# Kernel tuning notes

Hardware: AMD Instinct MI355X
Metric: run time of the kernel (lower is better)

The kernel has to match this reference:

```python
import jax, jax.numpy as jnp
import numpy as np

D_MODEL = 1024
D_STATE = 16
D_CONV = 4
EXPAND = 2
D_INNER = EXPAND * D_MODEL  # 2048
DT_MIN, DT_MAX = 0.001, 0.1
BATCH, SEQ = 4, 2048


def _silu(v):
    return v * jax.nn.sigmoid(v)


def setup_inputs() -> dict:
    key = jax.random.key(0)
    ks = jax.random.split(key, 5)
    x = jax.random.normal(ks[0], (BATCH, SEQ, D_MODEL), jnp.float32)
    W_in = jax.random.normal(ks[1], (2 * D_INNER, D_MODEL), jnp.float32) / np.sqrt(D_MODEL)
    conv_w = jax.random.normal(ks[2], (D_INNER, D_CONV), jnp.float32) / np.sqrt(D_CONV)
    conv_b = jnp.zeros((D_INNER,), jnp.float32)
    W_xproj = jax.random.normal(ks[3], (2 * D_STATE + 1, D_INNER), jnp.float32) / np.sqrt(D_INNER)
    A_log = jnp.log(jnp.arange(1, D_STATE + 1, dtype=jnp.float32))
    D_param = jnp.ones((D_INNER,), jnp.float32)
    W_out = jax.random.normal(ks[4], (D_MODEL, D_INNER), jnp.float32) / np.sqrt(D_INNER)
    return dict(x=x, W_in=W_in, conv_w=conv_w, conv_b=conv_b,
                W_xproj=W_xproj, A_log=A_log, D_param=D_param, W_out=W_out)


def reference(x, W_in, conv_w, conv_b, W_xproj, A_log, D_param, W_out):
    b, l, d = x.shape
    xz = x @ W_in.T                                   # (B, L, 2*d_inner)
    x_proj, z = jnp.split(xz, 2, axis=-1)             # each (B, L, d_inner)

    # Depthwise causal conv1d (kernel D_CONV, left-pad D_CONV-1, truncate to L)
    xp = jnp.pad(x_proj, ((0, 0), (D_CONV - 1, 0), (0, 0)))
    x_conv = conv_b + sum(xp[:, k:k + l, :] * conv_w[:, k] for k in range(D_CONV))
    x_conv = _silu(x_conv)                            # (B, L, d_inner)

    x_dbl = x_conv @ W_xproj.T                        # (B, L, 2*d_state+1)
    Bmat = x_dbl[..., :D_STATE]                       # (B, L, d_state)
    Cmat = x_dbl[..., D_STATE:2 * D_STATE]            # (B, L, d_state)
    dt = jnp.clip(jax.nn.softplus(x_dbl[..., -1]), DT_MIN, DT_MAX)  # (B, L)

    A = -jnp.exp(A_log)                               # (d_state,)

    def step(h, inp):
        x_t, dt_t, B_t, C_t = inp                     # (b,di), (b,), (b,ds), (b,ds)
        dt_A = jnp.clip(dt_t[:, None] * A, -20.0, 0.0)          # (b, ds)
        A_bar = jnp.exp(dt_A)[:, None, :]                        # (b, 1, ds)
        B_bar = jnp.clip(dt_t[:, None] * B_t, -10.0, 10.0)[:, None, :]
        h = jnp.clip(A_bar * h + B_bar * x_t[:, :, None], -100.0, 100.0)
        y_t = jnp.einsum('bds,bs->bd', h, C_t)
        return h, y_t

    h0 = jnp.zeros((b, D_INNER, D_STATE), x.dtype)
    xs = (jnp.swapaxes(x_conv, 0, 1), jnp.swapaxes(dt, 0, 1),
          jnp.swapaxes(Bmat, 0, 1), jnp.swapaxes(Cmat, 0, 1))
    _, ys = jax.lax.scan(step, h0, xs)                # ys: (L, B, d_inner)
    y = jnp.swapaxes(ys, 0, 1)                        # (B, L, d_inner)

    y = y * _silu(z) + x_conv * D_param
    return y @ W_out.T                                # (B, L, d_model)
```

## Files before the change

kernel.cpp:

```cpp
#include <hip/hip_runtime.h>
#include <cmath>

#define D_MODEL 1024
#define D_STATE 16
#define D_INNER 2048
#define NB 4
#define SEQL 2048
#define ROWS (NB*SEQL)
#define XZ_LD (2*D_INNER)

typedef __attribute__((ext_vector_type(8))) short short8;
typedef __attribute__((ext_vector_type(4))) float f32x4;

__device__ __forceinline__ float sigmoidf_(float v) { return 1.0f / (1.0f + __expf(-v)); }

__device__ __forceinline__ unsigned short bf16rne(float f) {
    unsigned u = __float_as_uint(f);
    unsigned r = (u + 0x7FFFu + ((u >> 16) & 1u)) >> 16;
    return (unsigned short)r;
}

__global__ __launch_bounds__(256) void pack1_k(const float4* __restrict__ in,
    ushort4* __restrict__ out, int n4)
{
    int i = blockIdx.x * 256 + threadIdx.x;
    if (i >= n4) return;
    float4 v = in[i];
    ushort4 h;
    h.x = bf16rne(v.x); h.y = bf16rne(v.y); h.z = bf16rne(v.z); h.w = bf16rne(v.w);
    out[i] = h;
}

#define GLDS(gp, lp) __builtin_amdgcn_global_load_lds( \
    (const __attribute__((address_space(1))) void*)(gp), \
    (__attribute__((address_space(3))) void*)(lp), 16, 0, 0)

extern __shared__ __align__(16) unsigned short smem8[];

template<int BM>
__global__ __launch_bounds__(512, 2) void gemm8p(
    const unsigned short* __restrict__ A2, int lda,
    const unsigned short* __restrict__ B2, int ldb,
    float* __restrict__ C, int ldc, int K)
{
    constexpr int APAN = BM * 32;
    constexpr int BPAN = 256 * 32;
    constexpr int LA   = BM / 128;
    constexpr int MH   = BM / 128;
    constexpr int WROW = (BM == 256) ? 128 : 64;
    unsigned short* sA = smem8;
    unsigned short* sB = smem8 + 3 * APAN;

    const int tid = threadIdx.x;
    const int bm = blockIdx.y * BM, bn = blockIdx.x * 256;
    const int wave = tid >> 6, lane = tid & 63;
    const int wm = wave >> 2, wn = wave & 3;
    const int fr = lane & 15, kq = lane >> 4;
    const int NT = K >> 5;

    size_t offA[LA], offB[2];
#pragma unroll
    for (int i = 0; i < LA; ++i) {
        int c = i * 512 + tid;
        int row = c & (BM - 1), slot = (BM == 256) ? (c >> 8) : (c >> 7);
        offA[i] = (size_t)(bm + row) * lda + slot * 8;
    }
#pragma unroll
    for (int i = 0; i < 2; ++i) {
        int c = i * 512 + tid;
        int row = c & 255, slot = c >> 8;
        offB[i] = (size_t)(bn + row) * ldb + slot * 8;
    }

    auto stageA = [&](int s) {
        int ka = s * 32;
        unsigned short* d = sA + (s % 3) * APAN;
#pragma unroll
        for (int i = 0; i < LA; ++i)
            GLDS(A2 + offA[i] + ka, d + (i * 512 + tid) * 8);
    };
    auto stageB = [&](int s) {
        int kb = s * 32;
        unsigned short* d = sB + (s % 3) * BPAN;
#pragma unroll
        for (int i = 0; i < 2; ++i)
            GLDS(B2 + offB[i] + kb, d + (i * 512 + tid) * 8);
    };

    f32x4 acc[4 * MH][4];
#pragma unroll
    for (int m = 0; m < 4 * MH; ++m)
#pragma unroll
        for (int n = 0; n < 4; ++n) acc[m][n] = (f32x4){0.f, 0.f, 0.f, 0.f};

    stageA(0); stageB(0); stageA(1); stageB(1);
    if constexpr (BM == 256) asm volatile("s_waitcnt vmcnt(4)" ::: "memory");
    else                     asm volatile("s_waitcnt vmcnt(3)" ::: "memory");
    __builtin_amdgcn_s_barrier();
    asm volatile("" ::: "memory");

    for (int t = 0; t < NT; ++t) {
        const unsigned short* pA = sA + (t % 3) * APAN;
        const unsigned short* pB = sB + (t % 3) * BPAN;
        short8 b0[4], a0[4];
#pragma unroll
        for (int n = 0; n < 4; ++n)
            b0[n] = *(const short8*)&pB[(kq * 256 + wn * 64 + n * 16 + fr) * 8];
#pragma unroll
        for (int m = 0; m < 4; ++m)
            a0[m] = *(const short8*)&pA[(kq * BM + wm * WROW + m * 16 + fr) * 8];
        if (t + 2 < NT) stageA(t + 2);
        if constexpr (MH == 1) { if (t + 2 < NT) stageB(t + 2); }
        __builtin_amdgcn_s_barrier();
        asm volatile("" ::: "memory");
        __builtin_amdgcn_s_setprio(1);
#pragma unroll
        for (int m = 0; m < 4; ++m)
#pragma unroll
            for (int n = 0; n < 4; ++n)
                acc[m][n] = __builtin_amdgcn_mfma_f32_16x16x32_bf16(a0[m], b0[n], acc[m][n], 0, 0, 0);
        __builtin_amdgcn_s_setprio(0);
        if constexpr (MH == 2) {
            __builtin_amdgcn_s_barrier();
            asm volatile("" ::: "memory");
            short8 a1[4];
#pragma unroll
            for (int m = 0; m < 4; ++m)
                a1[m] = *(const short8*)&pA[(kq * 256 + wm * 128 + 64 + m * 16 + fr) * 8];
            if (t + 2 < NT) stageB(t + 2);
            __builtin_amdgcn_s_barrier();
            asm volatile("" ::: "memory");
            __builtin_amdgcn_s_setprio(1);
#pragma unroll
            for (int m = 0; m < 4; ++m)
#pragma unroll
                for (int n = 0; n < 4; ++n)
                    acc[4 + m][n] = __builtin_amdgcn_mfma_f32_16x16x32_bf16(a1[m], b0[n], acc[4 + m][n], 0, 0, 0);
            __builtin_amdgcn_s_setprio(0);
        }
        if (t + 2 < NT) {
            if constexpr (BM == 256) asm volatile("s_waitcnt vmcnt(4)" ::: "memory");
            else                     asm volatile("s_waitcnt vmcnt(3)" ::: "memory");
        } else if (t + 1 < NT) {
            asm volatile("s_waitcnt vmcnt(0)" ::: "memory");
        }
        __builtin_amdgcn_s_barrier();
        asm volatile("" ::: "memory");
    }

#pragma unroll
    for (int mm = 0; mm < 4 * MH; ++mm) {
        int row0 = bm + wm * WROW + mm * 16 + kq * 4;
#pragma unroll
        for (int j = 0; j < 4; ++j) {
            float* Cr = C + (size_t)(row0 + j) * ldc + bn + wn * 64 + fr;
#pragma unroll
            for (int n = 0; n < 4; ++n) Cr[n * 16] = acc[mm][n][j];
        }
    }
}

__global__ __launch_bounds__(256) void conv_silu_k(
    const float* __restrict__ xz, const float* __restrict__ conv_w,
    const float* __restrict__ conv_b, float* __restrict__ x_conv)
{
    int idx = blockIdx.x * 256 + threadIdx.x;
    int q = idx & 511;
    int r = idx >> 9;
    int b = r >> 11, t = r & (SEQL - 1);
    int d0 = q << 2;
    float w[4][4];
#pragma unroll
    for (int c = 0; c < 4; ++c) *(float4*)w[c] = *(const float4*)&conv_w[(d0 + c) * 4];
    float4 acc = *(const float4*)&conv_b[d0];
    const float* xp = xz + (size_t)(b * SEQL) * XZ_LD + d0;
#pragma unroll
    for (int k = 0; k < 4; ++k) {
        int t2 = t - 3 + k;
        if (t2 >= 0) {
            float4 v = *(const float4*)(xp + (size_t)t2 * XZ_LD);
            acc.x = fmaf(v.x, w[0][k], acc.x);
            acc.y = fmaf(v.y, w[1][k], acc.y);
            acc.z = fmaf(v.z, w[2][k], acc.z);
            acc.w = fmaf(v.w, w[3][k], acc.w);
        }
    }
    acc.x *= sigmoidf_(acc.x);
    acc.y *= sigmoidf_(acc.y);
    acc.z *= sigmoidf_(acc.z);
    acc.w *= sigmoidf_(acc.w);
    *(float4*)&x_conv[(size_t)r * D_INNER + d0] = acc;
}

__global__ __launch_bounds__(256) void proj_k(
    const float* __restrict__ x_conv, const float* __restrict__ W_xproj,
    const float* __restrict__ A_log,
    float* __restrict__ Abar, float* __restrict__ Bbar, float* __restrict__ Cmat)
{
    __shared__ float sdbl[4][33];
    int tid = threadIdx.x;
    int w = tid >> 6, lane = tid & 63;
    int row = blockIdx.x * 4 + w;
    const float* xrow = x_conv + (size_t)row * D_INNER;
    float4 xr[8];
#pragma unroll
    for (int it = 0; it < 8; ++it)
        xr[it] = *(const float4*)&xrow[it * 256 + lane * 4];

    for (int j = 0; j < 33; ++j) {
        const float* wrow = W_xproj + j * D_INNER;
        float accv = 0.f;
#pragma unroll
        for (int it = 0; it < 8; ++it) {
            float4 wv = *(const float4*)&wrow[it * 256 + lane * 4];
            accv = fmaf(xr[it].x, wv.x, accv);
            accv = fmaf(xr[it].y, wv.y, accv);
            accv = fmaf(xr[it].z, wv.z, accv);
            accv = fmaf(xr[it].w, wv.w, accv);
        }
#pragma unroll
        for (int off = 32; off; off >>= 1) accv += __shfl_xor(accv, off);
        if (lane == 0) sdbl[w][j] = accv;
    }
    __syncthreads();
    if (tid < 64) {
        int w2 = tid >> 4, s = tid & 15;
        int row2 = blockIdx.x * 4 + w2;
        float draw = sdbl[w2][32];
        float sp = (draw > 20.f) ? draw : log1pf(__expf(draw));
        float dt = fminf(fmaxf(sp, 0.001f), 0.1f);
        float Aa = -__expf(A_log[s]);
        float dtA = fminf(fmaxf(dt * Aa, -20.f), 0.f);
        Abar[row2 * 16 + s] = __expf(dtA);
        float bb = dt * sdbl[w2][s];
        Bbar[row2 * 16 + s] = fminf(fmaxf(bb, -10.f), 10.f);
        Cmat[row2 * 16 + s] = sdbl[w2][16 + s];
    }
}

#define SCH 16
#define TT 16
__global__ __launch_bounds__(256) void scan_k(
    const float* __restrict__ x_conv, const float* __restrict__ xz,
    unsigned short* __restrict__ yhl,
    const float* __restrict__ Abar, const float* __restrict__ Bbar,
    const float* __restrict__ Cmat, const float* __restrict__ D_param)
{
    __shared__ __align__(16) float sXa[2][SCH][20];
    __shared__ float sZp[2][SCH][17];
    __shared__ __align__(16) float sPa[2][16][20];
    __shared__ __align__(16) float sPb[2][16][20];
    __shared__ __align__(16) float sPc[2][16][20];
    __shared__ __align__(16) float sT[SCH][328];

    const int tid = threadIdx.x;
    const int b = blockIdx.y, dbase = blockIdx.x * SCH;
    const int chl = tid >> 4, s = tid & 15;
    const float* xc = x_conv + (size_t)(b * SEQL) * D_INNER + dbase;
    const float* zp = xz + (size_t)(b * SEQL) * XZ_LD + D_INNER + dbase;
    const int pbase0 = (b * SEQL) * 16;
    const int st = tid >> 4, sc = tid & 15;

    auto stage = [&](int buf, int tc) {
        int t0 = tc * TT;
        sXa[buf][sc][st] = xc[(size_t)(t0 + st) * D_INNER + sc];
        sZp[buf][sc][st] = zp[(size_t)(t0 + st) * XZ_LD + sc];
        int g = pbase0 + t0 * 16 + tid;
        sPa[buf][sc][st] = Abar[g];
        sPb[buf][sc][st] = Bbar[g];
        sPc[buf][sc][st] = Cmat[g];
    };

    stage(0, 0);
    float h = 0.f;
    const float Dp = D_param[dbase + chl];

    for (int tc = 0; tc < SEQL / TT; ++tc) {
        int buf = tc & 1;
        int t0 = tc * TT;
        __syncthreads();
        if (tc + 1 < SEQL / TT) stage(buf ^ 1, tc + 1);

        float p[16];
#pragma unroll
        for (int q = 0; q < 4; ++q) {
            float4 a4 = *(const float4*)&sPa[buf][s][q * 4];
            float4 b4 = *(const float4*)&sPb[buf][s][q * 4];
            float4 c4 = *(const float4*)&sPc[buf][s][q * 4];
            float4 x4 = *(const float4*)&sXa[buf][chl][q * 4];
            h = fminf(fmaxf(fmaf(b4.x, x4.x, a4.x * h), -100.f), 100.f); p[q * 4 + 0] = h * c4.x;
            h = fminf(fmaxf(fmaf(b4.y, x4.y, a4.y * h), -100.f), 100.f); p[q * 4 + 1] = h * c4.y;
            h = fminf(fmaxf(fmaf(b4.z, x4.z, a4.z * h), -100.f), 100.f); p[q * 4 + 2] = h * c4.z;
            h = fminf(fmaxf(fmaf(b4.w, x4.w, a4.w * h), -100.f), 100.f); p[q * 4 + 3] = h * c4.w;
        }

#pragma unroll
        for (int i = 0; i < 16; ++i) sT[chl][i * 20 + s] = p[i];
        float4 r0 = *(const float4*)&sT[chl][s * 20 + 0];
        float4 r1 = *(const float4*)&sT[chl][s * 20 + 4];
        float4 r2 = *(const float4*)&sT[chl][s * 20 + 8];
        float4 r3 = *(const float4*)&sT[chl][s * 20 + 12];
        float ysum = ((r0.x + r1.x + r2.x + r3.x) + (r0.y + r1.y + r2.y + r3.y))
                   + ((r0.z + r1.z + r2.z + r3.z) + (r0.w + r1.w + r2.w + r3.w));

        float z = sZp[buf][chl][s];
        float x = sXa[buf][chl][s];
        float o = fmaf(x, Dp, ysum * (z * sigmoidf_(z)));
        size_t r = (size_t)(b * SEQL + t0 + s);
        yhl[r * 2 * XZ_LD + dbase + chl] = bf16rne(o);
    }
}

extern "C" void kernel_launch(void* const* d_in, const int* in_sizes, int n_in,
                              void* d_out, int out_size, void* d_ws, size_t ws_size,
                              hipStream_t stream) {
    const float* x       = (const float*)d_in[0];
    const float* W_in    = (const float*)d_in[1];
    const float* conv_w  = (const float*)d_in[2];
    const float* conv_b  = (const float*)d_in[3];
    const float* W_xproj = (const float*)d_in[4];
    const float* A_log   = (const float*)d_in[5];
    const float* D_param = (const float*)d_in[6];
    const float* W_out   = (const float*)d_in[7];
    float* out = (float*)d_out;

    char* p = (char*)d_ws;
    char* xzB = p;
    float* xz = (float*)xzB;
    p += (size_t)ROWS * XZ_LD * 4;
    char* xcB = p;
    float* x_conv = (float*)xcB;
    p += (size_t)ROWS * D_INNER * 4;
    float* Abar = (float*)p; p += (size_t)ROWS * 16 * 4;
    float* Bbar = (float*)p; p += (size_t)ROWS * 16 * 4;
    float* Cm   = (float*)p; p += (size_t)ROWS * 16 * 4;

    unsigned short* x1  = (unsigned short*)xcB;
    unsigned short* Wi1 = x1 + (size_t)ROWS * D_MODEL;
    unsigned short* Wo1 = (unsigned short*)xcB;
    unsigned short* yhl = (unsigned short*)xzB;

    constexpr int SM1 = (3 * 256 * 32 + 3 * 256 * 32) * 2;
    constexpr int SM2 = (3 * 128 * 32 + 3 * 256 * 32) * 2;

    pack1_k<<<ROWS * D_MODEL / 4 / 256, 256, 0, stream>>>(
        (const float4*)x, (ushort4*)x1, ROWS * D_MODEL / 4);
    pack1_k<<<2 * D_INNER * D_MODEL / 4 / 256, 256, 0, stream>>>(
        (const float4*)W_in, (ushort4*)Wi1, 2 * D_INNER * D_MODEL / 4);
    gemm8p<256><<<dim3(4096 / 256, ROWS / 256), 512, SM1, stream>>>(
        x1, D_MODEL, Wi1, D_MODEL, xz, XZ_LD, D_MODEL);
    conv_silu_k<<<ROWS * 512 / 256, 256, 0, stream>>>(xz, conv_w, conv_b, x_conv);
    proj_k<<<ROWS / 4, 256, 0, stream>>>(x_conv, W_xproj, A_log, Abar, Bbar, Cm);
    scan_k<<<dim3(D_INNER / SCH, NB), 256, 0, stream>>>(
        x_conv, xz, yhl, Abar, Bbar, Cm, D_param);
    pack1_k<<<D_MODEL * D_INNER / 4 / 256, 256, 0, stream>>>(
        (const float4*)W_out, (ushort4*)Wo1, D_MODEL * D_INNER / 4);
    gemm8p<128><<<dim3(1024 / 256, ROWS / 128), 512, SM2, stream>>>(
        yhl, 2 * XZ_LD, Wo1, D_INNER, out, D_MODEL, D_INNER);
}
```

Measured before the change: 488.0 us.

## Split selective scan into sequence segments with a carry-propagation pass

The sequential scan over 2048 timesteps is split into 16 segments run in parallel. A first pass computes each segment's end state and its cumulative decay product, a small carry kernel chains these across segments, and the main scan then restarts each segment from its carried-in state. This multiplies the number of scan blocks so the GPU is better occupied. The cost is an extra read of x_conv, Abar and Bbar plus two more launches. The carry combine treats the recurrence as linear and so ignores the ±100 clamp on h; the scratch values are stored in the now-unused x_proj half of the xz buffer.

After: 507.5 us. 4.0% more time.

```diff
diff --git a/kernel.cpp b/kernel.cpp
--- a/kernel.cpp
+++ b/kernel.cpp
@@ -238,10 +238,73 @@
     }
 }
 
+#define NSEG 16
+#define SLEN (SEQL / NSEG)
 #define SCH 16
 #define TT 16
+#define SEGC (SLEN / TT)
+#define SEGIDX(arr, f) ((size_t)((arr) * 2048 + ((f) >> 10)) * 4096 + 1024 + ((f) & 1023))
+
+__global__ __launch_bounds__(256) void scan_seg1(
+    const float* __restrict__ x_conv, float* __restrict__ xz,
+    const float* __restrict__ Abar, const float* __restrict__ Bbar)
+{
+    __shared__ __align__(16) float sXa[2][16][20];
+    __shared__ __align__(16) float sPa[2][16][20];
+    __shared__ __align__(16) float sPb[2][16][20];
+    const int tid = threadIdx.x;
+    const int b = blockIdx.y, dbase = blockIdx.x * SCH, seg = blockIdx.z;
+    const int chl = tid >> 4, s = tid & 15;
+    const float* xc = x_conv + ((size_t)(b * SEQL) + seg * SLEN) * D_INNER + dbase;
+    const int pbase0 = (b * SEQL + seg * SLEN) * 16;
+    const int st = tid >> 4, sc = tid & 15;
+
+    auto stage = [&](int buf, int tc) {
+        int t0 = tc * TT;
+        sXa[buf][sc][st] = xc[(size_t)(t0 + st) * D_INNER + sc];
+        int g = pbase0 + t0 * 16 + tid;
+        sPa[buf][sc][st] = Abar[g];
+        sPb[buf][sc][st] = Bbar[g];
+    };
+
+    stage(0, 0);
+    float h = 0.f, P = 1.f;
+
+    for (int tc = 0; tc < SEGC; ++tc) {
+        int buf = tc & 1;
+        __syncthreads();
+        if (tc + 1 < SEGC) stage(buf ^ 1, tc + 1);
+#pragma unroll
+        for (int q = 0; q < 4; ++q) {
+            float4 a4 = *(const float4*)&sPa[buf][s][q * 4];
+            float4 b4 = *(const float4*)&sPb[buf][s][q * 4];
+            float4 x4 = *(const float4*)&sXa[buf][chl][q * 4];
+            h = fminf(fmaxf(fmaf(b4.x, x4.x, a4.x * h), -100.f), 100.f); P *= a4.x;
+            h = fminf(fmaxf(fmaf(b4.y, x4.y, a4.y * h), -100.f), 100.f); P *= a4.y;
+            h = fminf(fmaxf(fmaf(b4.z, x4.z, a4.z * h), -100.f), 100.f); P *= a4.z;
+            h = fminf(fmaxf(fmaf(b4.w, x4.w, a4.w * h), -100.f), 100.f); P *= a4.w;
+        }
+    }
+    size_t f = ((size_t)(b * NSEG + seg) * D_INNER + dbase + chl) * 16 + s;
+    xz[SEGIDX(0, f)] = h;
+    xz[SEGIDX(1, f)] = P;
+}
+
+__global__ __launch_bounds__(256) void carry_k(float* __restrict__ xz)
+{
+    int idx = blockIdx.x * 256 + threadIdx.x;
+    int b = idx >> 15, ds = idx & 32767;
+    float c = 0.f;
+    xz[SEGIDX(2, (size_t)(b * NSEG) * 32768 + ds)] = 0.f;
+    for (int seg = 0; seg < NSEG - 1; ++seg) {
+        size_t f = (size_t)(b * NSEG + seg) * 32768 + ds;
+        c = xz[SEGIDX(1, f)] * c + xz[SEGIDX(0, f)];
+        xz[SEGIDX(2, f + 32768)] = c;
+    }
+}
+
 __global__ __launch_bounds__(256) void scan_k(
-    const float* __restrict__ x_conv, const float* __restrict__ xz,
+    const float* __restrict__ x_conv, float* __restrict__ xz,
     unsigned short* __restrict__ yhl,
     const float* __restrict__ Abar, const float* __restrict__ Bbar,
     const float* __restrict__ Cmat, const float* __restrict__ D_param)
@@ -254,11 +317,11 @@
     __shared__ __align__(16) float sT[SCH][328];
 
     const int tid = threadIdx.x;
-    const int b = blockIdx.y, dbase = blockIdx.x * SCH;
+    const int b = blockIdx.y, dbase = blockIdx.x * SCH, seg = blockIdx.z;
     const int chl = tid >> 4, s = tid & 15;
-    const float* xc = x_conv + (size_t)(b * SEQL) * D_INNER + dbase;
-    const float* zp = xz + (size_t)(b * SEQL) * XZ_LD + D_INNER + dbase;
-    const int pbase0 = (b * SEQL) * 16;
+    const float* xc = x_conv + ((size_t)(b * SEQL) + seg * SLEN) * D_INNER + dbase;
+    const float* zp = xz + ((size_t)(b * SEQL) + seg * SLEN) * XZ_LD + D_INNER + dbase;
+    const int pbase0 = (b * SEQL + seg * SLEN) * 16;
     const int st = tid >> 4, sc = tid & 15;
 
     auto stage = [&](int buf, int tc) {
@@ -272,14 +335,13 @@
     };
 
     stage(0, 0);
-    float h = 0.f;
+    float h = xz[SEGIDX(2, ((size_t)(b * NSEG + seg) * D_INNER + dbase + chl) * 16 + s)];
     const float Dp = D_param[dbase + chl];
 
-    for (int tc = 0; tc < SEQL / TT; ++tc) {
+    for (int tc = 0; tc < SEGC; ++tc) {
         int buf = tc & 1;
-        int t0 = tc * TT;
         __syncthreads();
-        if (tc + 1 < SEQL / TT) stage(buf ^ 1, tc + 1);
+        if (tc + 1 < SEGC) stage(buf ^ 1, tc + 1);
 
         float p[16];
 #pragma unroll
@@ -306,7 +368,7 @@
         float z = sZp[buf][chl][s];
         float x = sXa[buf][chl][s];
         float o = fmaf(x, Dp, ysum * (z * sigmoidf_(z)));
-        size_t r = (size_t)(b * SEQL + t0 + s);
+        size_t r = (size_t)(b * SEQL + seg * SLEN + tc * TT + s);
         yhl[r * 2 * XZ_LD + dbase + chl] = bf16rne(o);
     }
 }
@@ -351,7 +413,9 @@
         x1, D_MODEL, Wi1, D_MODEL, xz, XZ_LD, D_MODEL);
     conv_silu_k<<<ROWS * 512 / 256, 256, 0, stream>>>(xz, conv_w, conv_b, x_conv);
     proj_k<<<ROWS / 4, 256, 0, stream>>>(x_conv, W_xproj, A_log, Abar, Bbar, Cm);
-    scan_k<<<dim3(D_INNER / SCH, NB), 256, 0, stream>>>(
+    scan_seg1<<<dim3(D_INNER / SCH, NB, NSEG), 256, 0, stream>>>(x_conv, xz, Abar, Bbar);
+    carry_k<<<NB * 32768 / 256, 256, 0, stream>>>(xz);
+    scan_k<<<dim3(D_INNER / SCH, NB, NSEG), 256, 0, stream>>>(
         x_conv, xz, yhl, Abar, Bbar, Cm, D_param);
     pack1_k<<<D_MODEL * D_INNER / 4 / 256, 256, 0, stream>>>(
         (const float4*)W_out, (ushort4*)Wo1, D_MODEL * D_INNER / 4);
```
